# Kernel tuning notes

Measured on AMD Instinct MI355X. Metric: run time of the kernel, lower is better.

## Reference

```python
import jax, jax.numpy as jnp
import numpy as np


def setup_inputs() -> dict:
    key = jax.random.key(0)
    k1, k2, k3, k4, k5, k6 = jax.random.split(key, 6)
    B, C, H, W = 32, 512, 56, 56
    KD = 768
    x = jax.random.normal(k1, (B, C, H, W), dtype=jnp.float32)
    keyword = jax.random.normal(k2, (B, KD), dtype=jnp.float32)
    # Conv2d(2, 1, kernel_size=7): torch kaiming-uniform-ish init scale
    fan_in_conv = 2 * 7 * 7
    bnd_c = 1.0 / np.sqrt(fan_in_conv)
    conv_w = jax.random.uniform(k3, (1, 2, 7, 7), jnp.float32, -bnd_c, bnd_c)  # OIHW
    conv_b = jax.random.uniform(k4, (1,), jnp.float32, -bnd_c, bnd_c)
    # Linear(KD, 1)
    bnd_l = 1.0 / np.sqrt(KD)
    proj_w = jax.random.uniform(k5, (1, KD), jnp.float32, -bnd_l, bnd_l)
    proj_b = jax.random.uniform(k6, (1,), jnp.float32, -bnd_l, bnd_l)
    return {"x": x, "keyword": keyword, "conv_w": conv_w, "conv_b": conv_b,
            "proj_w": proj_w, "proj_b": proj_b}


def reference(x, keyword, conv_w, conv_b, proj_w, proj_b):
    # channel-wise max+mean pool -> [B, 2, H, W]
    x_compress = jnp.concatenate(
        [jnp.max(x, axis=1, keepdims=True), jnp.mean(x, axis=1, keepdims=True)],
        axis=1)
    # 7x7 conv, 2->1 channels, SAME padding (pad=3)
    attention = jax.lax.conv_general_dilated(
        x_compress, conv_w, window_strides=(1, 1), padding=[(3, 3), (3, 3)],
        dimension_numbers=("NCHW", "OIHW", "NCHW"))
    attention = attention + conv_b[None, :, None, None]  # [B,1,H,W]
    # keyword bias: Linear(KD->1), broadcast over H,W
    keyword_bias = keyword @ proj_w.T + proj_b  # [B,1]
    attention = attention + keyword_bias[:, :, None, None]
    scale = jax.nn.sigmoid(attention)
    return x * scale
```

## Files before the change

kernel.cpp:

```cpp
#include <hip/hip_runtime.h>
#include <math.h>

#define B 32
#define C 512
#define H 56
#define W 56
#define HW (H * W)
#define HW4 (HW / 4)
#define KD 768

__global__ __launch_bounds__(256) void pool_kernel(
    const float* __restrict__ x, float* __restrict__ cmax, float* __restrict__ cmean) {
    const int tid  = threadIdx.x;
    const int lane = tid & 63;
    const int cg   = tid >> 6;
    const int p    = blockIdx.x * 64 + lane;
    const int b    = p / HW4;
    const int hw4  = p - b * HW4;

    const float4* xb = (const float4*)x + (size_t)b * C * HW4 + hw4;

    float4 mx = make_float4(-INFINITY, -INFINITY, -INFINITY, -INFINITY);
    float4 sm = make_float4(0.f, 0.f, 0.f, 0.f);
    const int c0 = cg * (C / 4);
    #pragma unroll 4
    for (int c = c0; c < c0 + C / 4; ++c) {
        float4 v = xb[(size_t)c * HW4];
        mx.x = fmaxf(mx.x, v.x); mx.y = fmaxf(mx.y, v.y);
        mx.z = fmaxf(mx.z, v.z); mx.w = fmaxf(mx.w, v.w);
        sm.x += v.x; sm.y += v.y; sm.z += v.z; sm.w += v.w;
    }

    __shared__ float4 smax[4][64];
    __shared__ float4 ssum[4][64];
    smax[cg][lane] = mx;
    ssum[cg][lane] = sm;
    __syncthreads();

    if (cg == 0) {
        #pragma unroll
        for (int g = 1; g < 4; ++g) {
            float4 m2 = smax[g][lane];
            float4 s2 = ssum[g][lane];
            mx.x = fmaxf(mx.x, m2.x); mx.y = fmaxf(mx.y, m2.y);
            mx.z = fmaxf(mx.z, m2.z); mx.w = fmaxf(mx.w, m2.w);
            sm.x += s2.x; sm.y += s2.y; sm.z += s2.z; sm.w += s2.w;
        }
        const float inv = 1.0f / (float)C;
        float4 mn = make_float4(sm.x * inv, sm.y * inv, sm.z * inv, sm.w * inv);
        ((float4*)cmax)[p]  = mx;
        ((float4*)cmean)[p] = mn;
    }
}

__global__ __launch_bounds__(256) void bias_kernel(
    const float* __restrict__ keyword, const float* __restrict__ proj_w,
    const float* __restrict__ proj_b, float* __restrict__ bias) {
    const int b   = blockIdx.x;
    const int tid = threadIdx.x;
    float s = 0.f;
    for (int k = tid; k < KD; k += 256)
        s += keyword[b * KD + k] * proj_w[k];
    #pragma unroll
    for (int off = 32; off > 0; off >>= 1)
        s += __shfl_down(s, off);
    __shared__ float warp_s[4];
    if ((tid & 63) == 0) warp_s[tid >> 6] = s;
    __syncthreads();
    if (tid == 0)
        bias[b] = warp_s[0] + warp_s[1] + warp_s[2] + warp_s[3] + proj_b[0];
}

__global__ __launch_bounds__(256) void conv_kernel(
    const float* __restrict__ cmax, const float* __restrict__ cmean,
    const float* __restrict__ conv_w, const float* __restrict__ conv_b,
    const float* __restrict__ bias, float* __restrict__ scale) {
    __shared__ float wsm[98];
    __shared__ float cb;
    const int tid = threadIdx.x;
    if (tid < 98) wsm[tid] = conv_w[tid];
    if (tid == 98) cb = conv_b[0];
    __syncthreads();

    const int o  = blockIdx.x * 256 + tid;
    const int b  = o / HW;
    const int hw = o - b * HW;
    const int h  = hw / W;
    const int w  = hw - h * W;

    float acc = cb + bias[b];
    const float* cmx = cmax  + b * HW;
    const float* cmn = cmean + b * HW;
    #pragma unroll
    for (int kh = 0; kh < 7; ++kh) {
        const int ih = h + kh - 3;
        if (ih < 0 || ih >= H) continue;
        #pragma unroll
        for (int kw = 0; kw < 7; ++kw) {
            const int iw = w + kw - 3;
            if (iw < 0 || iw >= W) continue;
            const int idx = ih * W + iw;
            acc = fmaf(cmx[idx], wsm[kh * 7 + kw],
                  fmaf(cmn[idx], wsm[49 + kh * 7 + kw], acc));
        }
    }
    scale[o] = 1.0f / (1.0f + __expf(-acc));
}

__global__ __launch_bounds__(256) void scale_kernel(
    const float4* __restrict__ x4, const float4* __restrict__ scale4,
    float4* __restrict__ out4) {
    const int v    = blockIdx.x * 256 + threadIdx.x;
    const int rowv = v / HW4;
    const int hwv  = v - rowv * HW4;
    const int b    = rowv >> 9;
    float4 xv = x4[v];
    float4 sv = scale4[b * HW4 + hwv];
    out4[v] = make_float4(xv.x * sv.x, xv.y * sv.y, xv.z * sv.z, xv.w * sv.w);
}

extern "C" void kernel_launch(void* const* d_in, const int* in_sizes, int n_in,
                              void* d_out, int out_size, void* d_ws, size_t ws_size,
                              hipStream_t stream) {
    const float* x       = (const float*)d_in[0];
    const float* keyword = (const float*)d_in[1];
    const float* conv_w  = (const float*)d_in[2];
    const float* conv_b  = (const float*)d_in[3];
    const float* proj_w  = (const float*)d_in[4];
    const float* proj_b  = (const float*)d_in[5];
    float* out = (float*)d_out;

    float* ws    = (float*)d_ws;
    float* cmax  = ws;
    float* cmean = ws + B * HW;
    float* scale = ws + 2 * B * HW;
    float* bias  = ws + 3 * B * HW;

    pool_kernel<<<(B * HW4) / 64, 256, 0, stream>>>(x, cmax, cmean);
    bias_kernel<<<B, 256, 0, stream>>>(keyword, proj_w, proj_b, bias);
    conv_kernel<<<(B * HW) / 256, 256, 0, stream>>>(cmax, cmean, conv_w, conv_b, bias, scale);
    scale_kernel<<<(B * C * HW4) / 256, 256, 0, stream>>>(
        (const float4*)x, (const float4*)scale, (float4*)out);
}
```

Baseline: 396.1 us.

## Widen pool channel split, use nontemporal loads/stores and unroll scale kernel

Measured after the change: 391.4 us. Within noise of the previous version (-1.2%).

```diff
diff --git a/kernel.cpp b/kernel.cpp
--- a/kernel.cpp
+++ b/kernel.cpp
@@ -9,47 +9,51 @@
 #define HW4 (HW / 4)
 #define KD 768
 
-__global__ __launch_bounds__(256) void pool_kernel(
+typedef float floatx4 __attribute__((ext_vector_type(4)));
+
+__global__ __launch_bounds__(512) void pool_kernel(
     const float* __restrict__ x, float* __restrict__ cmax, float* __restrict__ cmean) {
-    const int tid  = threadIdx.x;
-    const int lane = tid & 63;
-    const int cg   = tid >> 6;
-    const int p    = blockIdx.x * 64 + lane;
-    const int b    = p / HW4;
-    const int hw4  = p - b * HW4;
+    const int tid = threadIdx.x;
+    const int pos = tid & 31;
+    const int cg  = tid >> 5;
+    const int p   = blockIdx.x * 32 + pos;
+    const int b   = p / HW4;
+    const int hw4 = p - b * HW4;
 
-    const float4* xb = (const float4*)x + (size_t)b * C * HW4 + hw4;
+    const floatx4* xb = (const floatx4*)x + (size_t)b * C * HW4 + hw4;
 
-    float4 mx = make_float4(-INFINITY, -INFINITY, -INFINITY, -INFINITY);
-    float4 sm = make_float4(0.f, 0.f, 0.f, 0.f);
-    const int c0 = cg * (C / 4);
+    floatx4 mx = { -INFINITY, -INFINITY, -INFINITY, -INFINITY };
+    floatx4 sm = { 0.f, 0.f, 0.f, 0.f };
+    const int c0 = cg * 32;
     #pragma unroll 4
-    for (int c = c0; c < c0 + C / 4; ++c) {
-        float4 v = xb[(size_t)c * HW4];
+    for (int c = c0; c < c0 + 32; ++c) {
+        floatx4 v = xb[(size_t)c * HW4];
         mx.x = fmaxf(mx.x, v.x); mx.y = fmaxf(mx.y, v.y);
         mx.z = fmaxf(mx.z, v.z); mx.w = fmaxf(mx.w, v.w);
-        sm.x += v.x; sm.y += v.y; sm.z += v.z; sm.w += v.w;
+        sm += v;
     }
 
-    __shared__ float4 smax[4][64];
-    __shared__ float4 ssum[4][64];
-    smax[cg][lane] = mx;
-    ssum[cg][lane] = sm;
+    __shared__ floatx4 smax[16][32];
+    __shared__ floatx4 ssum[16][32];
+    smax[cg][pos] = mx;
+    ssum[cg][pos] = sm;
     __syncthreads();
 
-    if (cg == 0) {
+    if (tid < 32) {
+        mx = smax[0][tid];
+        sm = ssum[0][tid];
         #pragma unroll
-        for (int g = 1; g < 4; ++g) {
-            float4 m2 = smax[g][lane];
-            float4 s2 = ssum[g][lane];
+        for (int g = 1; g < 16; ++g) {
+            floatx4 m2 = smax[g][tid];
             mx.x = fmaxf(mx.x, m2.x); mx.y = fmaxf(mx.y, m2.y);
             mx.z = fmaxf(mx.z, m2.z); mx.w = fmaxf(mx.w, m2.w);
-            sm.x += s2.x; sm.y += s2.y; sm.z += s2.z; sm.w += s2.w;
+            sm += ssum[g][tid];
         }
         const float inv = 1.0f / (float)C;
-        float4 mn = make_float4(sm.x * inv, sm.y * inv, sm.z * inv, sm.w * inv);
-        ((float4*)cmax)[p]  = mx;
-        ((float4*)cmean)[p] = mn;
+        floatx4 mn = sm * inv;
+        const int pp = blockIdx.x * 32 + tid;
+        ((floatx4*)cmax)[pp]  = mx;
+        ((floatx4*)cmean)[pp] = mn;
     }
 }
 
@@ -108,15 +112,20 @@
 }
 
 __global__ __launch_bounds__(256) void scale_kernel(
-    const float4* __restrict__ x4, const float4* __restrict__ scale4,
-    float4* __restrict__ out4) {
-    const int v    = blockIdx.x * 256 + threadIdx.x;
-    const int rowv = v / HW4;
-    const int hwv  = v - rowv * HW4;
-    const int b    = rowv >> 9;
-    float4 xv = x4[v];
-    float4 sv = scale4[b * HW4 + hwv];
-    out4[v] = make_float4(xv.x * sv.x, xv.y * sv.y, xv.z * sv.z, xv.w * sv.w);
+    const floatx4* __restrict__ x4, const floatx4* __restrict__ scale4,
+    floatx4* __restrict__ out4) {
+    const int base = blockIdx.x * 1024 + threadIdx.x;
+    #pragma unroll
+    for (int k = 0; k < 4; ++k) {
+        const int v    = base + k * 256;
+        const int rowv = v / HW4;
+        const int hwv  = v - rowv * HW4;
+        const int b    = rowv >> 9;
+        floatx4 xv = __builtin_nontemporal_load(&x4[v]);
+        floatx4 sv = scale4[b * HW4 + hwv];
+        floatx4 o  = xv * sv;
+        __builtin_nontemporal_store(o, &out4[v]);
+    }
 }
 
 extern "C" void kernel_launch(void* const* d_in, const int* in_sizes, int n_in,
@@ -136,9 +145,9 @@
     float* scale = ws + 2 * B * HW;
     float* bias  = ws + 3 * B * HW;
 
-    pool_kernel<<<(B * HW4) / 64, 256, 0, stream>>>(x, cmax, cmean);
     bias_kernel<<<B, 256, 0, stream>>>(keyword, proj_w, proj_b, bias);
+    pool_kernel<<<(B * HW4) / 32, 512, 0, stream>>>(x, cmax, cmean);
     conv_kernel<<<(B * HW) / 256, 256, 0, stream>>>(cmax, cmean, conv_w, conv_b, bias, scale);
-    scale_kernel<<<(B * C * HW4) / 256, 256, 0, stream>>>(
-        (const float4*)x, (const float4*)scale, (float4*)out);
+    scale_kernel<<<(B * C * HW4) / 1024, 256, 0, stream>>>(
+        (const floatx4*)x, (const floatx4*)scale, (float4*)out ? (floatx4*)out : (floatx4*)out);
 }
```
